# Performance work log

Measured on AMD Instinct MI355X. Metric: run time of the kernel, lower is better.

## Reference

```python
import jax, jax.numpy as jnp
import numpy as np

B, N, D, E = 4, 8192, 128, 262144


def setup_inputs() -> dict:
    key = jax.random.key(0)
    k_h, k_e, k_w1, k_b1, k_w2, k_b2 = jax.random.split(key, 6)
    h = jax.random.normal(k_h, (B, N, D), dtype=jnp.float32)
    edge_index = jax.random.randint(k_e, (2, E), 0, N, dtype=jnp.int64)
    # edge_mlp: Linear(2D -> D), SiLU, Linear(D -> 1). Kaiming-uniform-ish init scale.
    lim1 = 1.0 / np.sqrt(2 * D)
    lim2 = 1.0 / np.sqrt(D)
    W1 = jax.random.uniform(k_w1, (2 * D, D), minval=-lim1, maxval=lim1, dtype=jnp.float32)
    b1 = jax.random.uniform(k_b1, (D,), minval=-lim1, maxval=lim1, dtype=jnp.float32)
    W2 = jax.random.uniform(k_w2, (D, 1), minval=-lim2, maxval=lim2, dtype=jnp.float32)
    b2 = jax.random.uniform(k_b2, (1,), minval=-lim2, maxval=lim2, dtype=jnp.float32)
    return {"h": h, "edge_index": edge_index, "W1": W1, "b1": b1, "W2": W2, "b2": b2}


def reference(h, edge_index, W1, b1, W2, b2):
    # h: (B, N, D); edge_index: (2, E)
    src, dst = edge_index[0], edge_index[1]
    h_src = h[:, src, :]                                  # (B, E, D) gather
    h_dst = h[:, dst, :]                                  # (B, E, D) gather
    x = jnp.concatenate([h_src, h_dst], axis=-1)          # (B, E, 2D)
    hid = jax.nn.silu(jnp.einsum('bef,fd->bed', x, W1) + b1)  # (B, E, D)
    edge_scores = (jnp.einsum('bed,do->beo', hid, W2) + b2)[..., 0]  # (B, E)
    out = jnp.zeros((B, N, N), dtype=h.dtype)
    out = out.at[:, src, dst].set(edge_scores)            # scatter into dense (B, N, N)
    return out
```

## Files before the change

kernel.cpp:

```cpp
#include <hip/hip_runtime.h>
#include <hip/hip_bf16.h>
#include <stdint.h>

#define B_ 4
#define N_ 8192
#define D_ 128
#define E_ 262144

typedef __bf16 bf16x8 __attribute__((ext_vector_type(8)));
typedef unsigned short u16x8 __attribute__((ext_vector_type(8)));
typedef float f32x4 __attribute__((ext_vector_type(4)));

constexpr int BUCKET_CAP = 128;

constexpr size_t OFF_HB     = 0;
constexpr size_t OFF_BT     = 8388608;
constexpr size_t OFF_P      = 8454144;
constexpr size_t OFF_Q      = 16842752;
constexpr size_t OFF_SCORES = 25231360;
constexpr size_t OFF_CNT    = 29425664;
constexpr size_t OFF_BASE   = 29458432;
constexpr size_t OFF_BUCKET = 29491200;
constexpr size_t OFF_ORDER  = 33685504;

__device__ __forceinline__ unsigned short f2bf(float f) {
  union { float f; unsigned u; } v; v.f = f;
  unsigned r = v.u + 0x7fffu + ((v.u >> 16) & 1u);
  return (unsigned short)(r >> 16);
}
__device__ __forceinline__ float bf2f(unsigned short u) {
  return __uint_as_float((unsigned)u << 16);
}

__global__ void cast_h_k(const float* __restrict__ h, unsigned short* __restrict__ o) {
  int i = blockIdx.x * blockDim.x + threadIdx.x;
  float4 v = reinterpret_cast<const float4*>(h)[i];
  ushort4 r;
  r.x = f2bf(v.x); r.y = f2bf(v.y); r.z = f2bf(v.z); r.w = f2bf(v.w);
  reinterpret_cast<ushort4*>(o)[i] = r;
}

__global__ void bmat_k(const float* __restrict__ W1, unsigned short* __restrict__ o) {
  int i = blockIdx.x * blockDim.x + threadIdx.x;
  int dp = i >> 7, k = i & 127;
  int kk = (dp < 128) ? k : (128 + k);
  o[i] = f2bf(W1[kk * 128 + (dp & 127)]);
}

__global__ void place_k(const int* __restrict__ ei,
                        int* __restrict__ cnt, int* __restrict__ bucket) {
  int e = blockIdx.x * blockDim.x + threadIdx.x;
  int s = ei[e];
  int pos = atomicAdd(&cnt[s], 1);
  if (pos < BUCKET_CAP) bucket[s * BUCKET_CAP + pos] = e;
}

__global__ void prefix_k(const int* __restrict__ cnt, int* __restrict__ base) {
  __shared__ int sc[256];
  const int t = threadIdx.x;
  int c[32];
  int local = 0;
  #pragma unroll
  for (int j = 0; j < 32; ++j) {
    int v = cnt[t * 32 + j];
    v = v < BUCKET_CAP ? v : BUCKET_CAP;
    c[j] = v; local += v;
  }
  sc[t] = local;
  __syncthreads();
  #pragma unroll
  for (int off = 1; off < 256; off <<= 1) {
    int v = (t >= off) ? sc[t - off] : 0;
    __syncthreads();
    sc[t] += v;
    __syncthreads();
  }
  int run = sc[t] - local;
  #pragma unroll
  for (int j = 0; j < 32; ++j) { base[t * 32 + j] = run; run += c[j]; }
}

__global__ void order_build_k(const int* __restrict__ cnt, const int* __restrict__ base,
                              const int* __restrict__ bucket, int* __restrict__ order) {
  int s = blockIdx.x * blockDim.x + threadIdx.x;
  int n = cnt[s]; n = n < BUCKET_CAP ? n : BUCKET_CAP;
  int b0 = base[s];
  for (int j = 0; j < n; ++j) order[b0 + j] = bucket[s * BUCKET_CAP + j];
}

__global__ __launch_bounds__(512, 4) void proj_k(
    const unsigned short* __restrict__ hb,
    const unsigned short* __restrict__ bt,
    const float* __restrict__ b1,
    unsigned short* __restrict__ Pb,
    unsigned short* __restrict__ Qb) {
  __shared__ char lds[65536];
  const int tid  = threadIdx.x;
  const int lane = tid & 63;
  const int wid  = tid >> 6;
  const int l15  = lane & 15;
  const int lg   = lane >> 4;

  {
    const uint4* g = reinterpret_cast<const uint4*>(bt);
    #pragma unroll
    for (int it = 0; it < 8; ++it) {
      int i = it * 512 + tid;
      uint4 v = g[i];
      int byte = i * 16;
      int dd = byte >> 8;
      int within = byte & 255;
      *reinterpret_cast<uint4*>(&lds[dd * 256 + (within ^ ((dd & 7) << 4))]) = v;
    }
  }
  __syncthreads();

  const int r0 = blockIdx.x * 256 + wid * 32;
  const int kg = 8 * lg;

  bf16x8 a[2][4];
  #pragma unroll
  for (int m = 0; m < 2; ++m) {
    unsigned rowoff = (unsigned)(r0 + m * 16 + l15) * 128u;
    #pragma unroll
    for (int ks = 0; ks < 4; ++ks) {
      u16x8 u = *reinterpret_cast<const u16x8*>(hb + rowoff + ks * 32 + kg);
      a[m][ks] = __builtin_bit_cast(bf16x8, u);
    }
  }

  #pragma unroll
  for (int pass = 0; pass < 2; ++pass) {
    f32x4 acc[2][8];
    #pragma unroll
    for (int m = 0; m < 2; ++m)
      #pragma unroll
      for (int n = 0; n < 8; ++n)
        acc[m][n] = (f32x4){0.f, 0.f, 0.f, 0.f};

    #pragma unroll
    for (int ks = 0; ks < 4; ++ks) {
      const int kb = ks * 64 + 16 * lg;
      #pragma unroll
      for (int n = 0; n < 8; ++n) {
        int dd = pass * 128 + n * 16 + l15;
        uint4 v = *reinterpret_cast<const uint4*>(&lds[dd * 256 + (kb ^ ((dd & 7) << 4))]);
        bf16x8 bfr = __builtin_bit_cast(bf16x8, v);
        acc[0][n] = __builtin_amdgcn_mfma_f32_16x16x32_bf16(a[0][ks], bfr, acc[0][n], 0, 0, 0);
        acc[1][n] = __builtin_amdgcn_mfma_f32_16x16x32_bf16(a[1][ks], bfr, acc[1][n], 0, 0, 0);
      }
    }

    unsigned short* outp = pass == 0 ? Pb : Qb;
    #pragma unroll
    for (int m = 0; m < 2; ++m)
      #pragma unroll
      for (int n = 0; n < 8; ++n) {
        int col = n * 16 + l15;
        float bias = (pass == 0) ? b1[col] : 0.f;
        #pragma unroll
        for (int i = 0; i < 4; ++i) {
          int r = r0 + m * 16 + 4 * lg + i;
          outp[(unsigned)r * 128u + col] = f2bf(acc[m][n][i] + bias);
        }
      }
  }
}

__global__ __launch_bounds__(256, 8) void edge_score_k(
    const int* __restrict__ ei,
    const int* __restrict__ order,
    const unsigned short* __restrict__ Pb,
    const unsigned short* __restrict__ Qb,
    const float* __restrict__ w2,
    const float* __restrict__ b2,
    float* __restrict__ scores) {
  const int lane = threadIdx.x & 63;
  const int l15  = lane & 15;
  const int g    = lane >> 4;
  const int wv   = blockIdx.x * 4 + (threadIdx.x >> 6);
  const int nwav = gridDim.x * 4;

  float w2v[8];
  #pragma unroll
  for (int t = 0; t < 8; ++t) w2v[t] = w2[l15 * 8 + t];
  const float b2v = b2[0];
  const unsigned gbase = (unsigned)g * N_ * 128u + (unsigned)l15 * 8u;

  for (int c = wv * 4; c < E_; c += nwav * 4) {
    u16x8 pv[4], qv[4];
    int eidx[4];
    #pragma unroll
    for (int j = 0; j < 4; ++j) {
      int e = order[c + j];
      eidx[j] = e;
      unsigned s = (unsigned)ei[e];
      unsigned d = (unsigned)ei[E_ + e];
      pv[j] = *reinterpret_cast<const u16x8*>(Pb + gbase + s * 128u);
      qv[j] = *reinterpret_cast<const u16x8*>(Qb + gbase + d * 128u);
    }
    #pragma unroll
    for (int j = 0; j < 4; ++j) {
      float acc = 0.f;
      #pragma unroll
      for (int t = 0; t < 8; ++t) {
        float z = bf2f((unsigned short)pv[j][t]) + bf2f((unsigned short)qv[j][t]);
        float sv = z / (1.f + __expf(-z));
        acc += sv * w2v[t];
      }
      acc += __shfl_xor(acc, 1, 64);
      acc += __shfl_xor(acc, 2, 64);
      acc += __shfl_xor(acc, 4, 64);
      acc += __shfl_xor(acc, 8, 64);
      if (l15 == 0) scores[eidx[j] * 4 + g] = acc + b2v;
    }
  }
}

__global__ __launch_bounds__(256, 8) void out_writer_k(
    const int* __restrict__ ei,
    const int* __restrict__ cnt,
    const int* __restrict__ bucket,
    const f32x4* __restrict__ scores,
    float* __restrict__ out) {
  __shared__ int dst_l[BUCKET_CAP];
  __shared__ int e_l[BUCKET_CAP];
  __shared__ float sc4[BUCKET_CAP][4];
  __shared__ unsigned int idx32[2048];
  const int t = threadIdx.x;
  const int src = blockIdx.x;
  int n = cnt[src];
  n = n < BUCKET_CAP ? n : BUCKET_CAP;
  if (t < n) {
    int e = bucket[src * BUCKET_CAP + t];
    e_l[t] = e;
    dst_l[t] = ei[E_ + e];
    f32x4 s = scores[e];
    sc4[t][0] = s[0]; sc4[t][1] = s[1]; sc4[t][2] = s[2]; sc4[t][3] = s[3];
  }
  #pragma unroll
  for (int k = 0; k < 8; ++k) idx32[t + 256 * k] = 0u;
  __syncthreads();
  if (t < n) {
    int dst = dst_l[t], e = e_l[t];
    bool win = true;
    for (int j = 0; j < n; ++j)
      win = win && !(dst_l[j] == dst && e_l[j] > e);
    if (win) reinterpret_cast<unsigned char*>(idx32)[dst] = (unsigned char)(t + 1);
  }
  __syncthreads();

  const size_t rowbase = (size_t)src * N_;
  #pragma unroll
  for (int b = 0; b < 4; ++b) {
    f32x4* po = reinterpret_cast<f32x4*>(out + (size_t)b * ((size_t)N_ * N_) + rowbase);
    #pragma unroll
    for (int k = 0; k < 8; ++k) {
      int c = t + 256 * k;
      unsigned m4 = idx32[c];
      f32x4 v = (f32x4){0.f, 0.f, 0.f, 0.f};
      if (m4) {
        #pragma unroll
        for (int i = 0; i < 4; ++i) {
          unsigned mj = (m4 >> (8 * i)) & 255u;
          if (mj) v[i] = sc4[mj - 1][b];
        }
      }
      po[c] = v;
    }
  }
}

extern "C" void kernel_launch(void* const* d_in, const int* in_sizes, int n_in,
                              void* d_out, int out_size, void* d_ws, size_t ws_size,
                              hipStream_t stream) {
  const float* h  = (const float*)d_in[0];
  const int*   ei = (const int*)d_in[1];
  const float* W1 = (const float*)d_in[2];
  const float* b1 = (const float*)d_in[3];
  const float* W2 = (const float*)d_in[4];
  const float* b2 = (const float*)d_in[5];
  float* out = (float*)d_out;
  char*  ws  = (char*)d_ws;

  unsigned short* hb     = (unsigned short*)(ws + OFF_HB);
  unsigned short* bt     = (unsigned short*)(ws + OFF_BT);
  unsigned short* Pb     = (unsigned short*)(ws + OFF_P);
  unsigned short* Qb     = (unsigned short*)(ws + OFF_Q);
  float*          scores = (float*)(ws + OFF_SCORES);
  int*            cnt    = (int*)(ws + OFF_CNT);
  int*            base   = (int*)(ws + OFF_BASE);
  int*            bucket = (int*)(ws + OFF_BUCKET);
  int*            order  = (int*)(ws + OFF_ORDER);

  (void)hipMemsetAsync(cnt, 0, (size_t)N_ * 4, stream);
  (void)hipMemsetAsync(order, 0, (size_t)E_ * 4, stream);

  cast_h_k<<<4096, 256, 0, stream>>>(h, hb);
  bmat_k<<<128, 256, 0, stream>>>(W1, bt);
  place_k<<<E_ / 256, 256, 0, stream>>>(ei, cnt, bucket);
  prefix_k<<<1, 256, 0, stream>>>(cnt, base);
  order_build_k<<<32, 256, 0, stream>>>(cnt, base, bucket, order);
  proj_k<<<128, 512, 0, stream>>>(hb, bt, b1, Pb, Qb);
  edge_score_k<<<2048, 256, 0, stream>>>(ei, order, Pb, Qb, W2, b2, scores);
  out_writer_k<<<N_, 256, 0, stream>>>(ei, cnt, bucket, (const f32x4*)scores, out);
}
```

Before: 1.226 ms.

## Fuse edge scoring into per-source output writer, drop order build

New measurement: 1.134 ms. 1.08x faster.

```diff
diff --git a/kernel.cpp b/kernel.cpp
--- a/kernel.cpp
+++ b/kernel.cpp
@@ -17,11 +17,8 @@
 constexpr size_t OFF_BT     = 8388608;
 constexpr size_t OFF_P      = 8454144;
 constexpr size_t OFF_Q      = 16842752;
-constexpr size_t OFF_SCORES = 25231360;
-constexpr size_t OFF_CNT    = 29425664;
-constexpr size_t OFF_BASE   = 29458432;
-constexpr size_t OFF_BUCKET = 29491200;
-constexpr size_t OFF_ORDER  = 33685504;
+constexpr size_t OFF_CNT    = 25231360;
+constexpr size_t OFF_BUCKET = 25264128;
 
 __device__ __forceinline__ unsigned short f2bf(float f) {
   union { float f; unsigned u; } v; v.f = f;
@@ -53,39 +50,6 @@
   int s = ei[e];
   int pos = atomicAdd(&cnt[s], 1);
   if (pos < BUCKET_CAP) bucket[s * BUCKET_CAP + pos] = e;
-}
-
-__global__ void prefix_k(const int* __restrict__ cnt, int* __restrict__ base) {
-  __shared__ int sc[256];
-  const int t = threadIdx.x;
-  int c[32];
-  int local = 0;
-  #pragma unroll
-  for (int j = 0; j < 32; ++j) {
-    int v = cnt[t * 32 + j];
-    v = v < BUCKET_CAP ? v : BUCKET_CAP;
-    c[j] = v; local += v;
-  }
-  sc[t] = local;
-  __syncthreads();
-  #pragma unroll
-  for (int off = 1; off < 256; off <<= 1) {
-    int v = (t >= off) ? sc[t - off] : 0;
-    __syncthreads();
-    sc[t] += v;
-    __syncthreads();
-  }
-  int run = sc[t] - local;
-  #pragma unroll
-  for (int j = 0; j < 32; ++j) { base[t * 32 + j] = run; run += c[j]; }
-}
-
-__global__ void order_build_k(const int* __restrict__ cnt, const int* __restrict__ base,
-                              const int* __restrict__ bucket, int* __restrict__ order) {
-  int s = blockIdx.x * blockDim.x + threadIdx.x;
-  int n = cnt[s]; n = n < BUCKET_CAP ? n : BUCKET_CAP;
-  int b0 = base[s];
-  for (int j = 0; j < n; ++j) order[b0 + j] = bucket[s * BUCKET_CAP + j];
 }
 
 __global__ __launch_bounds__(512, 4) void proj_k(
@@ -167,61 +131,14 @@
   }
 }
 
-__global__ __launch_bounds__(256, 8) void edge_score_k(
+__global__ __launch_bounds__(256, 8) void out_writer_k(
     const int* __restrict__ ei,
-    const int* __restrict__ order,
+    const int* __restrict__ cnt,
+    const int* __restrict__ bucket,
     const unsigned short* __restrict__ Pb,
     const unsigned short* __restrict__ Qb,
     const float* __restrict__ w2,
     const float* __restrict__ b2,
-    float* __restrict__ scores) {
-  const int lane = threadIdx.x & 63;
-  const int l15  = lane & 15;
-  const int g    = lane >> 4;
-  const int wv   = blockIdx.x * 4 + (threadIdx.x >> 6);
-  const int nwav = gridDim.x * 4;
-
-  float w2v[8];
-  #pragma unroll
-  for (int t = 0; t < 8; ++t) w2v[t] = w2[l15 * 8 + t];
-  const float b2v = b2[0];
-  const unsigned gbase = (unsigned)g * N_ * 128u + (unsigned)l15 * 8u;
-
-  for (int c = wv * 4; c < E_; c += nwav * 4) {
-    u16x8 pv[4], qv[4];
-    int eidx[4];
-    #pragma unroll
-    for (int j = 0; j < 4; ++j) {
-      int e = order[c + j];
-      eidx[j] = e;
-      unsigned s = (unsigned)ei[e];
-      unsigned d = (unsigned)ei[E_ + e];
-      pv[j] = *reinterpret_cast<const u16x8*>(Pb + gbase + s * 128u);
-      qv[j] = *reinterpret_cast<const u16x8*>(Qb + gbase + d * 128u);
-    }
-    #pragma unroll
-    for (int j = 0; j < 4; ++j) {
-      float acc = 0.f;
-      #pragma unroll
-      for (int t = 0; t < 8; ++t) {
-        float z = bf2f((unsigned short)pv[j][t]) + bf2f((unsigned short)qv[j][t]);
-        float sv = z / (1.f + __expf(-z));
-        acc += sv * w2v[t];
-      }
-      acc += __shfl_xor(acc, 1, 64);
-      acc += __shfl_xor(acc, 2, 64);
-      acc += __shfl_xor(acc, 4, 64);
-      acc += __shfl_xor(acc, 8, 64);
-      if (l15 == 0) scores[eidx[j] * 4 + g] = acc + b2v;
-    }
-  }
-}
-
-__global__ __launch_bounds__(256, 8) void out_writer_k(
-    const int* __restrict__ ei,
-    const int* __restrict__ cnt,
-    const int* __restrict__ bucket,
-    const f32x4* __restrict__ scores,
     float* __restrict__ out) {
   __shared__ int dst_l[BUCKET_CAP];
   __shared__ int e_l[BUCKET_CAP];
@@ -235,12 +152,40 @@
     int e = bucket[src * BUCKET_CAP + t];
     e_l[t] = e;
     dst_l[t] = ei[E_ + e];
-    f32x4 s = scores[e];
-    sc4[t][0] = s[0]; sc4[t][1] = s[1]; sc4[t][2] = s[2]; sc4[t][3] = s[3];
   }
   #pragma unroll
   for (int k = 0; k < 8; ++k) idx32[t + 256 * k] = 0u;
   __syncthreads();
+
+  {
+    const int l16 = t & 15;
+    const int G   = t >> 4;
+    const int b   = G & 3;
+    float w2v[8];
+    #pragma unroll
+    for (int u = 0; u < 8; ++u) w2v[u] = w2[l16 * 8 + u];
+    const float b2v = b2[0];
+    const unsigned gbase = ((unsigned)b * N_) * 128u + (unsigned)l16 * 8u;
+    u16x8 pv = *reinterpret_cast<const u16x8*>(Pb + gbase + (unsigned)src * 128u);
+    for (int j = G >> 2; j < n; j += 4) {
+      unsigned dst = (unsigned)dst_l[j];
+      u16x8 qv = *reinterpret_cast<const u16x8*>(Qb + gbase + dst * 128u);
+      float acc = 0.f;
+      #pragma unroll
+      for (int u = 0; u < 8; ++u) {
+        float z = bf2f((unsigned short)pv[u]) + bf2f((unsigned short)qv[u]);
+        float sv = z / (1.f + __expf(-z));
+        acc += sv * w2v[u];
+      }
+      acc += __shfl_xor(acc, 1, 64);
+      acc += __shfl_xor(acc, 2, 64);
+      acc += __shfl_xor(acc, 4, 64);
+      acc += __shfl_xor(acc, 8, 64);
+      if (l16 == 0) sc4[j][b] = acc + b2v;
+    }
+  }
+  __syncthreads();
+
   if (t < n) {
     int dst = dst_l[t], e = e_l[t];
     bool win = true;
@@ -287,21 +232,14 @@
   unsigned short* bt     = (unsigned short*)(ws + OFF_BT);
   unsigned short* Pb     = (unsigned short*)(ws + OFF_P);
   unsigned short* Qb     = (unsigned short*)(ws + OFF_Q);
-  float*          scores = (float*)(ws + OFF_SCORES);
   int*            cnt    = (int*)(ws + OFF_CNT);
-  int*            base   = (int*)(ws + OFF_BASE);
   int*            bucket = (int*)(ws + OFF_BUCKET);
-  int*            order  = (int*)(ws + OFF_ORDER);
 
   (void)hipMemsetAsync(cnt, 0, (size_t)N_ * 4, stream);
-  (void)hipMemsetAsync(order, 0, (size_t)E_ * 4, stream);
 
   cast_h_k<<<4096, 256, 0, stream>>>(h, hb);
   bmat_k<<<128, 256, 0, stream>>>(W1, bt);
   place_k<<<E_ / 256, 256, 0, stream>>>(ei, cnt, bucket);
-  prefix_k<<<1, 256, 0, stream>>>(cnt, base);
-  order_build_k<<<32, 256, 0, stream>>>(cnt, base, bucket, order);
   proj_k<<<128, 512, 0, stream>>>(hb, bt, b1, Pb, Qb);
-  edge_score_k<<<2048, 256, 0, stream>>>(ei, order, Pb, Qb, W2, b2, scores);
-  out_writer_k<<<N_, 256, 0, stream>>>(ei, cnt, bucket, (const f32x4*)scores, out);
-}
+  out_writer_k<<<N_, 256, 0, stream>>>(ei, cnt, bucket, Pb, Qb, W2, b2, out);
+}
```
